# Kernel tuning notes

Measured on AMD Instinct MI355X. Metric: run time of the kernel, lower is better.

The kernel has to match this reference:

```python
import jax, jax.numpy as jnp
import numpy as np
import math

Z_DIM = 1024
DOWN = 512
UP = 1024
HEADS = 16
ROPE_HD = 64
HEAD_DIM = Z_DIM // HEADS  # 64, used only in softmax scale
V_HD = UP // HEADS


def _rope(x, num_heads, head_dim, base=10000.0):
    # x: [bs, L, num_heads*head_dim] -> [bs, num_heads, L, head_dim]
    bs, L, _ = x.shape
    theta = 1.0 / (base ** (jnp.arange(0, head_dim, 2, dtype=jnp.float32) / head_dim))
    pe = jnp.arange(L, dtype=jnp.float32)[:, None] * theta[None, :]  # [L, hd/2]
    # NOTE: faithful to source, which stores sin(pos) in cos_pos and cos(pos) in sin_pos
    cos_pos = jnp.repeat(jnp.sin(pe), 2, axis=-1)  # [L, hd]
    sin_pos = jnp.repeat(jnp.cos(pe), 2, axis=-1)
    q = x.reshape(bs, L, num_heads, head_dim).transpose(0, 2, 1, 3)
    q2 = jnp.stack([-q[..., 1::2], q[..., ::2]], axis=-1).reshape(q.shape)
    return q * cos_pos + q2 * sin_pos


def setup_inputs() -> dict:
    key = jax.random.key(0)
    ks = jax.random.split(key, 20)
    B, S = 2, 2048
    s = lambda fan_in: 1.0 / math.sqrt(fan_in)
    d = {
        'query': jax.random.normal(ks[0], (B, S, Z_DIM), jnp.float32),
        'key': jax.random.normal(ks[1], (B, S, Z_DIM), jnp.float32),
        'value': jax.random.normal(ks[2], (B, S, Z_DIM), jnp.float32),
        'w_dkv': jax.random.uniform(ks[3], (Z_DIM, DOWN), jnp.float32, -s(Z_DIM), s(Z_DIM)),
        'b_dkv': jnp.zeros((DOWN,), jnp.float32),
        'w_uk': jax.random.uniform(ks[4], (DOWN, UP), jnp.float32, -s(DOWN), s(DOWN)),
        'b_uk': jnp.zeros((UP,), jnp.float32),
        'w_uv': jax.random.uniform(ks[5], (DOWN, UP), jnp.float32, -s(DOWN), s(DOWN)),
        'b_uv': jnp.zeros((UP,), jnp.float32),
        'w_dq': jax.random.uniform(ks[6], (Z_DIM, DOWN), jnp.float32, -s(Z_DIM), s(Z_DIM)),
        'b_dq': jnp.zeros((DOWN,), jnp.float32),
        'w_uq': jax.random.uniform(ks[7], (DOWN, UP), jnp.float32, -s(DOWN), s(DOWN)),
        'b_uq': jnp.zeros((UP,), jnp.float32),
        'w_qr': jax.random.uniform(ks[8], (DOWN, ROPE_HD * HEADS), jnp.float32, -s(DOWN), s(DOWN)),
        'b_qr': jnp.zeros((ROPE_HD * HEADS,), jnp.float32),
        'w_kr': jax.random.uniform(ks[9], (Z_DIM, ROPE_HD), jnp.float32, -s(Z_DIM), s(Z_DIM)),
        'b_kr': jnp.zeros((ROPE_HD,), jnp.float32),
        'w_fc': jax.random.uniform(ks[10], (HEADS * V_HD, Z_DIM), jnp.float32, -s(HEADS * V_HD), s(HEADS * V_HD)),
        'b_fc': jnp.zeros((Z_DIM,), jnp.float32),
    }
    return d


def reference(query, key, value, w_dkv, b_dkv, w_uk, b_uk, w_uv, b_uv,
              w_dq, b_dq, w_uq, b_uq, w_qr, b_qr, w_kr, b_kr, w_fc, b_fc):
    bs, S, _ = query.shape
    c_t_kv = key @ w_dkv + b_dkv                      # [B,S,down]
    k_t_c = c_t_kv @ w_uk + b_uk                      # [B,S,up]
    v_t_c = c_t_kv @ w_uv + b_uv                      # [B,S,up]
    c_t_q = query @ w_dq + b_dq                       # [B,S,down]
    q_t_c = c_t_q @ w_uq + b_uq                       # [B,S,up]
    q_t_r = _rope(c_t_q @ w_qr + b_qr, HEADS, ROPE_HD)  # [B,H,S,rope_hd]
    k_t_r = _rope(key @ w_kr + b_kr, 1, ROPE_HD)         # [B,1,S,rope_hd]

    q_t_c = q_t_c.reshape(bs, S, HEADS, V_HD).transpose(0, 2, 1, 3)  # [B,H,S,dc]
    q = jnp.concatenate([q_t_c, q_t_r], axis=-1)                      # [B,H,S,dc+dr]
    k_t_c = k_t_c.reshape(bs, S, HEADS, V_HD).transpose(0, 2, 1, 3)
    k = jnp.concatenate([k_t_c, jnp.broadcast_to(k_t_r, (bs, HEADS, S, ROPE_HD))], axis=-1)

    scores = jnp.einsum('bhqd,bhkd->bhqk', q, k)
    scale = math.sqrt(HEAD_DIM) + math.sqrt(ROPE_HD)
    attn = jax.nn.softmax(scores / scale, axis=-1)    # dropout is identity (eval / p=0)

    v = v_t_c.reshape(bs, S, HEADS, V_HD).transpose(0, 2, 1, 3)
    out = jnp.einsum('bhqk,bhkd->bhqd', attn, v)      # [B,H,S,v_hd]
    out = out.transpose(0, 2, 1, 3).reshape(bs, S, HEADS * V_HD)
    return out @ w_fc + b_fc
```

## Files before the change

### kernel.cpp

```cpp
#include <hip/hip_runtime.h>
#include <hip/hip_bf16.h>
#include <hip/hip_fp16.h>

typedef __attribute__((ext_vector_type(8))) short    bf16x8;
typedef __attribute__((ext_vector_type(4))) float    f32x4;
typedef __attribute__((ext_vector_type(4))) _Float16 f16x4;
typedef __attribute__((ext_vector_type(2))) __fp16   fp16x2_raw;

typedef const void __attribute__((address_space(1))) gvoid_t;
typedef void __attribute__((address_space(3)))       lvoid_t;

static __device__ __forceinline__ void gload_lds16(const void* g, void* l) {
    __builtin_amdgcn_global_load_lds((gvoid_t*)g, (lvoid_t*)l, 16, 0, 0);
}

static __device__ __forceinline__ short bfbits(float f) {
    union { __hip_bfloat16 h; short s; } u;
    u.h = __float2bfloat16(f);
    return u.s;
}

__global__ __launch_bounds__(256) void cvt_bf16_dual(const float* __restrict__ q,
                                                     const float* __restrict__ k,
                                                     __hip_bfloat16* __restrict__ qd,
                                                     __hip_bfloat16* __restrict__ kd, int n8) {
    int t = blockIdx.x * 256 + threadIdx.x;
    const float* src;
    __hip_bfloat16* dst;
    int i;
    if (t < n8)          { src = q; dst = qd; i = t; }
    else if (t < 2 * n8) { src = k; dst = kd; i = t - n8; }
    else return;
    float4 a = ((const float4*)src)[2 * i];
    float4 b = ((const float4*)src)[2 * i + 1];
    bf16x8 o;
    o[0] = bfbits(a.x); o[1] = bfbits(a.y); o[2] = bfbits(a.z); o[3] = bfbits(a.w);
    o[4] = bfbits(b.x); o[5] = bfbits(b.y); o[6] = bfbits(b.z); o[7] = bfbits(b.w);
    ((bf16x8*)dst)[i] = o;
}

struct TJob { const float* src; __hip_bfloat16* dst; int K, N, tx; };
struct TJobPack { TJob j[8]; int start[8]; };

__global__ __launch_bounds__(256) void transpose_cvt_batch(TJobPack P) {
    __shared__ __hip_bfloat16 tile[64][72];
    const int bid = blockIdx.x;
    int ji = 0;
#pragma unroll
    for (int k = 1; k < 8; ++k) if (bid >= P.start[k]) ji = k;
    const TJob J = P.j[ji];
    const int local = bid - P.start[ji];
    const int kb = (local % J.tx) * 64;
    const int nb = (local / J.tx) * 64;
    const int c  = threadIdx.x & 63;
    const int r0 = threadIdx.x >> 6;
    if (nb < J.N) {
#pragma unroll
        for (int i = 0; i < 16; ++i) {
            int r = r0 + i * 4;
            tile[r][c] = __float2bfloat16(J.src[(size_t)(kb + r) * J.N + nb + c]);
        }
        __syncthreads();
#pragma unroll
        for (int i = 0; i < 16; ++i) {
            int r = r0 + i * 4;
            J.dst[(size_t)(nb + r) * J.K + kb + c] = tile[c][r];
        }
    } else {
        __hip_bfloat16 z = __float2bfloat16(0.0f);
#pragma unroll
        for (int i = 0; i < 16; ++i) {
            int r = r0 + i * 4;
            J.dst[(size_t)(nb + r) * J.K + kb + c] = z;
        }
    }
}

__global__ __launch_bounds__(256) void bias_prep(const float* __restrict__ b_dkv, const float* __restrict__ b_kr,
                                                 const float* __restrict__ b_uk,  const float* __restrict__ b_uv,
                                                 const float* __restrict__ b_uq,  const float* __restrict__ b_qr,
                                                 float* __restrict__ bcat1, float* __restrict__ bcat2,
                                                 float* __restrict__ bcat3) {
    int t = blockIdx.x * 256 + threadIdx.x;
    if (t < 640) {
        bcat1[t] = (t < 512) ? b_dkv[t] : ((t - 512) < 64 ? b_kr[t - 512] : 0.0f);
    } else if (t < 2688) {
        int u = t - 640;
        bcat2[u] = (u < 1024) ? b_uq[u] : b_qr[u - 1024];
    } else if (t < 4736) {
        int u = t - 2688;
        bcat3[u] = (u < 1024) ? b_uk[u] : b_uv[u - 1024];
    }
}

struct GJob {
    const __hip_bfloat16* A; const __hip_bfloat16* Bt; const float* bias;
    void* C0; void* C1; int N, K, lda, ldb, ldc; float scale; int mode;
};

__global__ __launch_bounds__(256) void gemm_dual(GJob j0, GJob j1, int split) {
    __shared__ __align__(16) __hip_bfloat16 sA[2][64 * 32];
    __shared__ __align__(16) __hip_bfloat16 sB[2][128 * 32];
    const GJob J  = (blockIdx.x < (unsigned)split) ? j0 : j1;
    const int bx  = (blockIdx.x < (unsigned)split) ? blockIdx.x : blockIdx.x - split;
    const int tid  = threadIdx.x;
    const int wid  = tid >> 6;
    const int lane = tid & 63;
    const int lr   = lane & 15;
    const int lg   = lane >> 4;
    const int mb   = blockIdx.y * 64;
    const int nb   = bx * 128;
    const int wr   = (wid >> 1) * 32;
    const int wc   = (wid & 1) * 64;

    auto stage = [&](int bufi, int k0) {
        {
            int e   = wid * 512 + lane * 8;
            int row = e >> 5, col = e & 31;
            gload_lds16(J.A + (size_t)(mb + row) * J.lda + (k0 + col), &sA[bufi][wid * 512]);
        }
#pragma unroll
        for (int j = 0; j < 2; ++j) {
            int cb  = wid * 2 + j;
            int e   = cb * 512 + lane * 8;
            int row = e >> 5, col = e & 31;
            gload_lds16(J.Bt + (size_t)(nb + row) * J.ldb + (k0 + col), &sB[bufi][cb * 512]);
        }
    };

    f32x4 acc[2][4] = {};
    const int nt = J.K / 32;
    stage(0, 0);
    asm volatile("s_waitcnt vmcnt(0)" ::: "memory");
    __syncthreads();

    for (int t = 0; t < nt; ++t) {
        const int cur = t & 1;
        if (t + 1 < nt) stage(cur ^ 1, (t + 1) * 32);
        bf16x8 af[2], bfr[4];
#pragma unroll
        for (int m = 0; m < 2; ++m)
            af[m] = *(const bf16x8*)&sA[cur][(wr + m * 16 + lr) * 32 + lg * 8];
#pragma unroll
        for (int n = 0; n < 4; ++n)
            bfr[n] = *(const bf16x8*)&sB[cur][(wc + n * 16 + lr) * 32 + lg * 8];
#pragma unroll
        for (int m = 0; m < 2; ++m)
#pragma unroll
            for (int n = 0; n < 4; ++n)
                acc[m][n] = __builtin_amdgcn_mfma_f32_16x16x32_bf16(af[m], bfr[n], acc[m][n], 0, 0, 0);
        asm volatile("s_waitcnt vmcnt(0)" ::: "memory");
        __syncthreads();
    }

#pragma unroll
    for (int n = 0; n < 4; ++n) {
        int col  = nb + wc + n * 16 + lr;
        float bv = J.bias ? J.bias[col] : 0.0f;
#pragma unroll
        for (int m = 0; m < 2; ++m) {
#pragma unroll
            for (int r = 0; r < 4; ++r) {
                int row    = mb + wr + m * 16 + lg * 4 + r;
                float val  = (acc[m][n][r] + bv) * J.scale;
                if (J.mode == 1) ((float*)J.C0)[(size_t)row * J.ldc + col] = val;
                else             ((__hip_bfloat16*)J.C0)[(size_t)row * J.ldc + col] = __float2bfloat16(val);
            }
        }
    }
}

__global__ __launch_bounds__(256) void gemm128_dual(GJob j0, GJob j1, int split) {
    __shared__ __align__(16) __hip_bfloat16 sA[2][128 * 32];
    __shared__ __align__(16) __hip_bfloat16 sB[2][128 * 32];
    const GJob J  = (blockIdx.x < (unsigned)split) ? j0 : j1;
    const int bx  = (blockIdx.x < (unsigned)split) ? blockIdx.x : blockIdx.x - split;
    const int tid  = threadIdx.x;
    const int wid  = tid >> 6;
    const int lane = tid & 63;
    const int lr   = lane & 15;
    const int lg   = lane >> 4;
    const int mb   = blockIdx.y * 128;
    const int nb   = bx * 128;
    const int wr   = (wid >> 1) * 64;
    const int wc   = (wid & 1) * 64;

    auto stage = [&](int bufi, int k0) {
#pragma unroll
        for (int j = 0; j < 2; ++j) {
            int c   = wid * 2 + j;
            int e   = c * 512 + lane * 8;
            int row = e >> 5, col = e & 31;
            gload_lds16(J.A + (size_t)(mb + row) * J.lda + (k0 + col), &sA[bufi][c * 512]);
        }
#pragma unroll
        for (int j = 0; j < 2; ++j) {
            int c   = wid * 2 + j;
            int e   = c * 512 + lane * 8;
            int row = e >> 5, col = e & 31;
            gload_lds16(J.Bt + (size_t)(nb + row) * J.ldb + (k0 + col), &sB[bufi][c * 512]);
        }
    };

    f32x4 acc[4][4] = {};
    const int nt = J.K / 32;
    stage(0, 0);
    asm volatile("s_waitcnt vmcnt(0)" ::: "memory");
    __syncthreads();

    for (int t = 0; t < nt; ++t) {
        const int cur = t & 1;
        if (t + 1 < nt) stage(cur ^ 1, (t + 1) * 32);
        bf16x8 af[4], bfr[4];
#pragma unroll
        for (int m = 0; m < 4; ++m)
            af[m] = *(const bf16x8*)&sA[cur][(wr + m * 16 + lr) * 32 + lg * 8];
#pragma unroll
        for (int n = 0; n < 4; ++n)
            bfr[n] = *(const bf16x8*)&sB[cur][(wc + n * 16 + lr) * 32 + lg * 8];
#pragma unroll
        for (int m = 0; m < 4; ++m)
#pragma unroll
            for (int n = 0; n < 4; ++n)
                acc[m][n] = __builtin_amdgcn_mfma_f32_16x16x32_bf16(af[m], bfr[n], acc[m][n], 0, 0, 0);
        asm volatile("s_waitcnt vmcnt(0)" ::: "memory");
        __syncthreads();
    }

#pragma unroll
    for (int n = 0; n < 4; ++n) {
        int col  = nb + wc + n * 16 + lr;
        float bv = J.bias ? J.bias[col] : 0.0f;
#pragma unroll
        for (int m = 0; m < 4; ++m) {
#pragma unroll
            for (int r = 0; r < 4; ++r) {
                int row    = mb + wr + m * 16 + lg * 4 + r;
                float val  = (acc[m][n][r] + bv) * J.scale;
                if (J.mode == 3) {
                    if (col < 1024) ((__hip_bfloat16*)J.C0)[(size_t)row * 1024 + col] = __float2bfloat16(val);
                    else            ((_Float16*)J.C1)[(size_t)row * 1024 + col - 1024] = (_Float16)val;
                } else {
                    ((__hip_bfloat16*)J.C0)[(size_t)row * J.ldc + col] = __float2bfloat16(val);
                }
            }
        }
    }
}

__global__ __launch_bounds__(256) void misc_kernel(const _Float16* __restrict__ vtc,
                                                   _Float16* __restrict__ vtcT,
                                                   __hip_bfloat16* __restrict__ qrope,
                                                   __hip_bfloat16* __restrict__ krope,
                                                   int R, int S) {
    __shared__ _Float16 tile[64][72];
    const int tp  = R >> 2;
    const int bid = blockIdx.x;
    if (bid < tp) {
        const int cb = (bid % 16) * 64;
        const int rb = (bid / 16) * 64;
        const int c4 = (threadIdx.x & 15) * 4;
        const int rl = threadIdx.x >> 4;
#pragma unroll
        for (int i = 0; i < 4; ++i) {
            int row = rl + i * 16;
            *(f16x4*)&tile[row][c4] = *(const f16x4*)&vtc[(size_t)(rb + row) * 1024 + cb + c4];
        }
        __syncthreads();
#pragma unroll
        for (int i = 0; i < 4; ++i) {
            int orow = rl + i * 16;
            f16x4 v;
#pragma unroll
            for (int j = 0; j < 4; ++j) v[j] = tile[c4 + j][orow];
            *(f16x4*)&vtcT[(size_t)(cb + orow) * R + rb + c4] = v;
        }
        return;
    }
    int t = (bid - tp) * 256 + threadIdx.x;
    const int nq = R * 512;
    __hip_bfloat16* x;
    int i, row, rowstride, hh;
    if (t < nq)               { i = t & 31; hh = (t >> 5) & 15; row = t >> 9; x = qrope; rowstride = 2048; }
    else if (t < nq + R * 32) { t -= nq; i = t & 31; hh = 0; row = t >> 5; x = krope; rowstride = 640; }
    else return;
    int pos = row % S;
    float theta = __expf(-0.28782313662425572f * (float)i);
    float pe = (float)pos * theta;
    float sp, cp;
    sincosf(pe, &sp, &cp);
    size_t idx = (size_t)row * rowstride + hh * 64 + 2 * i;
    float x0 = __bfloat162float(x[idx]);
    float x1 = __bfloat162float(x[idx + 1]);
    x[idx]     = __float2bfloat16(x0 * sp - x1 * cp);
    x[idx + 1] = __float2bfloat16(x1 * sp + x0 * cp);
}

__global__ __launch_bounds__(256, 2) void attn_kernel(const __hip_bfloat16* __restrict__ qcat,
                                                      const __hip_bfloat16* __restrict__ ktc,
                                                      const __hip_bfloat16* __restrict__ kr,
                                                      const _Float16* __restrict__ vtcT,
                                                      __hip_bfloat16* __restrict__ outp,
                                                      int S, int R) {
    __shared__ __align__(16) char lds[2][24 * 1024];
    const int tid  = threadIdx.x;
    const int wid  = tid >> 6;
    const int lane = tid & 63;
    const int lr   = lane & 15;
    const int lg   = lane >> 4;

    const int NQ   = S / 128;
    const int L    = blockIdx.x;
    const int slot = L >> 3;
    const int gg   = (L & 7) + 8 * (slot / NQ);
    const int qt   = slot % NQ;
    const int h    = gg & 15;
    const int b    = gg >> 4;
    const size_t base = (size_t)b * S;
    const int qb   = qt * 128 + wid * 32;

    auto stage = [&](int bufi, int kt) {
        char* bufK = lds[bufi];
        char* bufV = lds[bufi] + 16 * 1024;
#pragma unroll
        for (int j = 0; j < 4; ++j) {
            int c   = wid * 4 + j;
            int rho = c * 4 + (lane >> 4);
            int u   = (lane & 15) ^ (rho & 15);
            const __hip_bfloat16* src = (u < 8)
                ? ktc + (base + kt + rho) * 1024 + h * 64 + u * 8
                : kr  + (base + kt + rho) * 640 + (u & 7) * 8;
            gload_lds16(src, bufK + c * 1024);
        }
#pragma unroll
        for (int j = 0; j < 2; ++j) {
            int c   = wid * 2 + j;
            int rho = c * 8 + (lane >> 3);
            int u   = (lane & 7) ^ (rho & 7);
            gload_lds16(vtcT + (size_t)(h * 64 + rho) * R + base + kt + u * 8,
                        bufV + c * 1024);
        }
    };

    bf16x8 qf[2][4];
#pragma unroll
    for (int g = 0; g < 2; ++g) {
        size_t row = base + qb + g * 16 + lr;
        const __hip_bfloat16* pq = qcat + row * 2048 + h * 64;
        qf[g][0] = *(const bf16x8*)(pq + lg * 8);
        qf[g][1] = *(const bf16x8*)(pq + 32 + lg * 8);
        qf[g][2] = *(const bf16x8*)(pq + 1024 + lg * 8);
        qf[g][3] = *(const bf16x8*)(pq + 1024 + 32 + lg * 8);
    }

    f32x4 oacc[2][4] = {};
    float lrun[2] = {0.0f, 0.0f};

    const int NT = S / 64;
    stage(0, 0);
    __syncthreads();

    for (int t = 0; t < NT; ++t) {
        const int cur = t & 1;
        if (t + 1 < NT) stage(cur ^ 1, (t + 1) * 64);

        const char* bufK = lds[cur];
        const char* bufV = lds[cur] + 16 * 1024;

        f32x4 sacc[2][4] = {};
#pragma unroll
        for (int st = 0; st < 4; ++st) {
            bf16x8 kf[4];
#pragma unroll
            for (int c = 0; c < 4; ++c)
                kf[c] = *(const bf16x8*)(bufK + (st * 16 + lr) * 256 +
                                         (((c * 4 + lg) ^ lr) << 4));
#pragma unroll
            for (int g = 0; g < 2; ++g)
#pragma unroll
                for (int c = 0; c < 4; ++c)
                    sacc[g][st] = __builtin_amdgcn_mfma_f32_16x16x32_bf16(kf[c], qf[g][c], sacc[g][st], 0, 0, 0);
        }

        f16x4 vf[4][4];
#pragma unroll
        for (int st = 0; st < 4; ++st)
#pragma unroll
            for (int vt = 0; vt < 4; ++vt)
                vf[st][vt] = *(const f16x4*)(bufV + (vt * 16 + lr) * 128 +
                                             (((st * 2 + (lg >> 1)) ^ (lr & 7)) << 4) + (lg & 1) * 8);

#pragma unroll
        for (int g = 0; g < 2; ++g) {
            float p[4][4];
#pragma unroll
            for (int st = 0; st < 4; ++st)
#pragma unroll
                for (int r = 0; r < 4; ++r) {
                    p[st][r] = __builtin_exp2f(sacc[g][st][r]);
                    lrun[g] += p[st][r];
                }
#pragma unroll
            for (int st = 0; st < 4; ++st) {
                union { fp16x2_raw h2[2]; f16x4 v; } pu;
                pu.h2[0] = __builtin_amdgcn_cvt_pkrtz(p[st][0], p[st][1]);
                pu.h2[1] = __builtin_amdgcn_cvt_pkrtz(p[st][2], p[st][3]);
#pragma unroll
                for (int vt = 0; vt < 4; ++vt)
                    oacc[g][vt] = __builtin_amdgcn_mfma_f32_16x16x16f16(vf[st][vt], pu.v, oacc[g][vt], 0, 0, 0);
            }
        }
        __syncthreads();
    }

#pragma unroll
    for (int g = 0; g < 2; ++g) {
        lrun[g] += __shfl_xor(lrun[g], 16);
        lrun[g] += __shfl_xor(lrun[g], 32);
        float inv = 1.0f / lrun[g];
        size_t rowoff = (base + qb + g * 16 + lr) << 10;
#pragma unroll
        for (int vt = 0; vt < 4; ++vt)
#pragma unroll
            for (int r = 0; r < 4; ++r)
                outp[rowoff + h * 64 + vt * 16 + lg * 4 + r] =
                    __float2bfloat16(oacc[g][vt][r] * inv);
    }
}

extern "C" void kernel_launch(void* const* d_in, const int* in_sizes, int n_in,
                              void* d_out, int out_size, void* d_ws, size_t ws_size,
                              hipStream_t stream) {
    const float* query = (const float*)d_in[0];
    const float* key   = (const float*)d_in[1];
    const float* w_dkv = (const float*)d_in[3];
    const float* b_dkv = (const float*)d_in[4];
    const float* w_uk  = (const float*)d_in[5];
    const float* b_uk  = (const float*)d_in[6];
    const float* w_uv  = (const float*)d_in[7];
    const float* b_uv  = (const float*)d_in[8];
    const float* w_dq  = (const float*)d_in[9];
    const float* b_dq  = (const float*)d_in[10];
    const float* w_uq  = (const float*)d_in[11];
    const float* b_uq  = (const float*)d_in[12];
    const float* w_qr  = (const float*)d_in[13];
    const float* b_qr  = (const float*)d_in[14];
    const float* w_kr  = (const float*)d_in[15];
    const float* b_kr  = (const float*)d_in[16];
    const float* w_fc  = (const float*)d_in[17];
    const float* b_fc  = (const float*)d_in[18];

    const int B = 2;
    const int R = in_sizes[0] / 1024;
    const int S = R / B;
    const float QSCALE = 1.4426950408889634f / 16.0f;

    char* ws = (char*)d_ws;
    size_t off = 0;
    auto alloc = [&](size_t bytes) -> char* {
        char* p = ws + off;
        off += (bytes + 255) & ~(size_t)255;
        return p;
    };

    __hip_bfloat16* q_bf  = (__hip_bfloat16*)alloc((size_t)R * 1024 * 2);
    __hip_bfloat16* k_bf  = (__hip_bfloat16*)alloc((size_t)R * 1024 * 2);
    __hip_bfloat16* wcat1 = (__hip_bfloat16*)alloc(640 * 1024 * 2);
    __hip_bfloat16* wdq_t = (__hip_bfloat16*)alloc(512 * 1024 * 2);
    __hip_bfloat16* wcat3 = (__hip_bfloat16*)alloc(2048 * 512 * 2);
    __hip_bfloat16* wcat2 = (__hip_bfloat16*)alloc(2048 * 512 * 2);
    __hip_bfloat16* wfc_t = (__hip_bfloat16*)alloc(1024 * 1024 * 2);
    float*          bcat1 = (float*)alloc(640 * 4);
    float*          bcat2 = (float*)alloc(2048 * 4);
    float*          bcat3 = (float*)alloc(2048 * 4);
    __hip_bfloat16* ckkr  = (__hip_bfloat16*)alloc((size_t)R * 640 * 2);
    __hip_bfloat16* c_q   = (__hip_bfloat16*)alloc((size_t)R * 512 * 2);
    __hip_bfloat16* ktc   = (__hip_bfloat16*)alloc((size_t)R * 1024 * 2);
    _Float16*       vtc   = (_Float16*)alloc((size_t)R * 1024 * 2);
    _Float16*       vtcT  = (_Float16*)alloc((size_t)R * 1024 * 2);
    __hip_bfloat16* qcat  = (__hip_bfloat16*)alloc((size_t)R * 2048 * 2);
    __hip_bfloat16* attn_out = q_bf;

    cvt_bf16_dual<<<dim3(2 * R * 1024 / 8 / 256), 256, 0, stream>>>(query, key, q_bf, k_bf, R * 1024 / 8);

    TJobPack P;
    P.j[0] = {w_dkv, wcat1,              1024, 512,  16};
    P.j[1] = {w_kr,  wcat1 + 512 * 1024, 1024, 64,   16};
    P.j[2] = {w_dq,  wdq_t,              1024, 512,  16};
    P.j[3] = {w_uk,  wcat3,              512,  1024, 8};
    P.j[4] = {w_uv,  wcat3 + 1024 * 512, 512,  1024, 8};
    P.j[5] = {w_uq,  wcat2,              512,  1024, 8};
    P.j[6] = {w_qr,  wcat2 + 1024 * 512, 512,  1024, 8};
    P.j[7] = {w_fc,  wfc_t,              1024, 1024, 16};
    int st = 0;
    const int counts[8] = {128, 32, 128, 128, 128, 128, 128, 256};
    for (int i = 0; i < 8; ++i) { P.start[i] = st; st += counts[i]; }
    transpose_cvt_batch<<<dim3(st), 256, 0, stream>>>(P);

    bias_prep<<<dim3(19), 256, 0, stream>>>(b_dkv, b_kr, b_uk, b_uv, b_uq, b_qr, bcat1, bcat2, bcat3);

    GJob ja0 = {k_bf, wcat1, bcat1, ckkr, nullptr, 640, 1024, 1024, 1024, 640, 1.0f, 0};
    GJob ja1 = {q_bf, wdq_t, b_dq,  c_q,  nullptr, 512, 1024, 1024, 1024, 512, 1.0f, 0};
    gemm_dual<<<dim3(9, R / 64), 256, 0, stream>>>(ja0, ja1, 5);

    GJob jb0 = {ckkr, wcat3, bcat3, ktc,  vtc,     2048, 512, 640, 512, 1024, 1.0f,   3};
    GJob jb1 = {c_q,  wcat2, bcat2, qcat, nullptr, 2048, 512, 512, 512, 2048, QSCALE, 0};
    gemm128_dual<<<dim3(32, R / 128), 256, 0, stream>>>(jb0, jb1, 16);

    {
        int tp = R >> 2;
        int ropeBlocks = (R * 512 + R * 32 + 255) / 256;
        misc_kernel<<<dim3(tp + ropeBlocks), 256, 0, stream>>>(vtc, vtcT, qcat + 1024, ckkr + 512, R, S);
    }

    attn_kernel<<<dim3((S / 128) * 16 * B), 256, 0, stream>>>(qcat, ktc, ckkr + 512, vtcT, attn_out, S, R);

    GJob jc0 = {attn_out, wfc_t, b_fc, d_out, nullptr, 1024, 1024, 1024, 1024, 1024, 1.0f, 1};
    gemm_dual<<<dim3(8, R / 64), 256, 0, stream>>>(jc0, jc0, 8);
}
```

Measured before the change: 187.7 us.

## Fuse V transpose into up-projection GEMM epilogue via LDS staging

The up-projection GEMM now transposes the V output tile through shared memory in its epilogue and writes vtcT directly with vectorized stores. This removes the intermediate vtc buffer and the transpose part of the misc kernel, saving one full read and write of V. The rope kernel also switches to fast __sincosf and a bitmask for the position, assuming S is a power of two. The fast sincos may lose some accuracy for large arguments.

```diff
diff --git a/kernel.cpp b/kernel.cpp
--- a/kernel.cpp
+++ b/kernel.cpp
@@ -5,6 +5,7 @@
 typedef __attribute__((ext_vector_type(8))) short    bf16x8;
 typedef __attribute__((ext_vector_type(4))) float    f32x4;
 typedef __attribute__((ext_vector_type(4))) _Float16 f16x4;
+typedef __attribute__((ext_vector_type(8))) _Float16 f16x8;
 typedef __attribute__((ext_vector_type(2))) __fp16   fp16x2_raw;
 
 typedef const void __attribute__((address_space(1))) gvoid_t;
@@ -170,9 +171,10 @@
     }
 }
 
-__global__ __launch_bounds__(256) void gemm128_dual(GJob j0, GJob j1, int split) {
-    __shared__ __align__(16) __hip_bfloat16 sA[2][128 * 32];
-    __shared__ __align__(16) __hip_bfloat16 sB[2][128 * 32];
+__global__ __launch_bounds__(256) void gemm128_dual(GJob j0, GJob j1, int split, int Rtot) {
+    __shared__ __align__(16) char smem[128 * 132 * 2];
+    __hip_bfloat16* sA = (__hip_bfloat16*)smem;
+    __hip_bfloat16* sB = (__hip_bfloat16*)(smem + 16384);
     const GJob J  = (blockIdx.x < (unsigned)split) ? j0 : j1;
     const int bx  = (blockIdx.x < (unsigned)split) ? blockIdx.x : blockIdx.x - split;
     const int tid  = threadIdx.x;
@@ -191,14 +193,14 @@
             int c   = wid * 2 + j;
             int e   = c * 512 + lane * 8;
             int row = e >> 5, col = e & 31;
-            gload_lds16(J.A + (size_t)(mb + row) * J.lda + (k0 + col), &sA[bufi][c * 512]);
+            gload_lds16(J.A + (size_t)(mb + row) * J.lda + (k0 + col), &sA[bufi * 4096 + c * 512]);
         }
 #pragma unroll
         for (int j = 0; j < 2; ++j) {
             int c   = wid * 2 + j;
             int e   = c * 512 + lane * 8;
             int row = e >> 5, col = e & 31;
-            gload_lds16(J.Bt + (size_t)(nb + row) * J.ldb + (k0 + col), &sB[bufi][c * 512]);
+            gload_lds16(J.Bt + (size_t)(nb + row) * J.ldb + (k0 + col), &sB[bufi * 4096 + c * 512]);
         }
     };
 
@@ -214,10 +216,10 @@
         bf16x8 af[4], bfr[4];
 #pragma unroll
         for (int m = 0; m < 4; ++m)
-            af[m] = *(const bf16x8*)&sA[cur][(wr + m * 16 + lr) * 32 + lg * 8];
+            af[m] = *(const bf16x8*)&sA[cur * 4096 + (wr + m * 16 + lr) * 32 + lg * 8];
 #pragma unroll
         for (int n = 0; n < 4; ++n)
-            bfr[n] = *(const bf16x8*)&sB[cur][(wc + n * 16 + lr) * 32 + lg * 8];
+            bfr[n] = *(const bf16x8*)&sB[cur * 4096 + (wc + n * 16 + lr) * 32 + lg * 8];
 #pragma unroll
         for (int m = 0; m < 4; ++m)
 #pragma unroll
@@ -227,6 +229,30 @@
         __syncthreads();
     }
 
+    if (J.mode == 3 && nb >= 1024) {
+        _Float16* T = (_Float16*)smem;
+#pragma unroll
+        for (int n = 0; n < 4; ++n) {
+            int cl = wc + n * 16 + lr;
+            float bv = J.bias[nb + cl];
+#pragma unroll
+            for (int m = 0; m < 4; ++m)
+#pragma unroll
+                for (int r = 0; r < 4; ++r)
+                    T[cl * 132 + wr + m * 16 + lg * 4 + r] =
+                        (_Float16)((acc[m][n][r] + bv) * J.scale);
+        }
+        __syncthreads();
+        const int vd   = tid >> 1;
+        const int half = tid & 1;
+        _Float16* dst = (_Float16*)J.C1 + (size_t)(nb - 1024 + vd) * Rtot + mb + half * 64;
+        const _Float16* srcT = T + vd * 132 + half * 64;
+#pragma unroll
+        for (int j = 0; j < 8; ++j)
+            *(f16x8*)&dst[j * 8] = *(const f16x8*)&srcT[j * 8];
+        return;
+    }
+
 #pragma unroll
     for (int n = 0; n < 4; ++n) {
         int col  = nb + wc + n * 16 + lr;
@@ -237,58 +263,28 @@
             for (int r = 0; r < 4; ++r) {
                 int row    = mb + wr + m * 16 + lg * 4 + r;
                 float val  = (acc[m][n][r] + bv) * J.scale;
-                if (J.mode == 3) {
-                    if (col < 1024) ((__hip_bfloat16*)J.C0)[(size_t)row * 1024 + col] = __float2bfloat16(val);
-                    else            ((_Float16*)J.C1)[(size_t)row * 1024 + col - 1024] = (_Float16)val;
-                } else {
-                    ((__hip_bfloat16*)J.C0)[(size_t)row * J.ldc + col] = __float2bfloat16(val);
-                }
+                if (J.mode == 3) ((__hip_bfloat16*)J.C0)[(size_t)row * 1024 + col] = __float2bfloat16(val);
+                else             ((__hip_bfloat16*)J.C0)[(size_t)row * J.ldc + col] = __float2bfloat16(val);
             }
         }
     }
 }
 
-__global__ __launch_bounds__(256) void misc_kernel(const _Float16* __restrict__ vtc,
-                                                   _Float16* __restrict__ vtcT,
-                                                   __hip_bfloat16* __restrict__ qrope,
+__global__ __launch_bounds__(256) void rope_kernel(__hip_bfloat16* __restrict__ qrope,
                                                    __hip_bfloat16* __restrict__ krope,
                                                    int R, int S) {
-    __shared__ _Float16 tile[64][72];
-    const int tp  = R >> 2;
-    const int bid = blockIdx.x;
-    if (bid < tp) {
-        const int cb = (bid % 16) * 64;
-        const int rb = (bid / 16) * 64;
-        const int c4 = (threadIdx.x & 15) * 4;
-        const int rl = threadIdx.x >> 4;
-#pragma unroll
-        for (int i = 0; i < 4; ++i) {
-            int row = rl + i * 16;
-            *(f16x4*)&tile[row][c4] = *(const f16x4*)&vtc[(size_t)(rb + row) * 1024 + cb + c4];
-        }
-        __syncthreads();
-#pragma unroll
-        for (int i = 0; i < 4; ++i) {
-            int orow = rl + i * 16;
-            f16x4 v;
-#pragma unroll
-            for (int j = 0; j < 4; ++j) v[j] = tile[c4 + j][orow];
-            *(f16x4*)&vtcT[(size_t)(cb + orow) * R + rb + c4] = v;
-        }
-        return;
-    }
-    int t = (bid - tp) * 256 + threadIdx.x;
+    int t = blockIdx.x * 256 + threadIdx.x;
     const int nq = R * 512;
     __hip_bfloat16* x;
     int i, row, rowstride, hh;
     if (t < nq)               { i = t & 31; hh = (t >> 5) & 15; row = t >> 9; x = qrope; rowstride = 2048; }
     else if (t < nq + R * 32) { t -= nq; i = t & 31; hh = 0; row = t >> 5; x = krope; rowstride = 640; }
     else return;
-    int pos = row % S;
+    int pos = row & (S - 1);
     float theta = __expf(-0.28782313662425572f * (float)i);
     float pe = (float)pos * theta;
     float sp, cp;
-    sincosf(pe, &sp, &cp);
+    __sincosf(pe, &sp, &cp);
     size_t idx = (size_t)row * rowstride + hh * 64 + 2 * i;
     float x0 = __bfloat162float(x[idx]);
     float x1 = __bfloat162float(x[idx + 1]);
@@ -476,7 +472,6 @@
     __hip_bfloat16* ckkr  = (__hip_bfloat16*)alloc((size_t)R * 640 * 2);
     __hip_bfloat16* c_q   = (__hip_bfloat16*)alloc((size_t)R * 512 * 2);
     __hip_bfloat16* ktc   = (__hip_bfloat16*)alloc((size_t)R * 1024 * 2);
-    _Float16*       vtc   = (_Float16*)alloc((size_t)R * 1024 * 2);
     _Float16*       vtcT  = (_Float16*)alloc((size_t)R * 1024 * 2);
     __hip_bfloat16* qcat  = (__hip_bfloat16*)alloc((size_t)R * 2048 * 2);
     __hip_bfloat16* attn_out = q_bf;
@@ -503,15 +498,11 @@
     GJob ja1 = {q_bf, wdq_t, b_dq,  c_q,  nullptr, 512, 1024, 1024, 1024, 512, 1.0f, 0};
     gemm_dual<<<dim3(9, R / 64), 256, 0, stream>>>(ja0, ja1, 5);
 
-    GJob jb0 = {ckkr, wcat3, bcat3, ktc,  vtc,     2048, 512, 640, 512, 1024, 1.0f,   3};
+    GJob jb0 = {ckkr, wcat3, bcat3, ktc,  vtcT,    2048, 512, 640, 512, 1024, 1.0f,   3};
     GJob jb1 = {c_q,  wcat2, bcat2, qcat, nullptr, 2048, 512, 512, 512, 2048, QSCALE, 0};
-    gemm128_dual<<<dim3(32, R / 128), 256, 0, stream>>>(jb0, jb1, 16);
-
-    {
-        int tp = R >> 2;
-        int ropeBlocks = (R * 512 + R * 32 + 255) / 256;
-        misc_kernel<<<dim3(tp + ropeBlocks), 256, 0, stream>>>(vtc, vtcT, qcat + 1024, ckkr + 512, R, S);
-    }
+    gemm128_dual<<<dim3(32, R / 128), 256, 0, stream>>>(jb0, jb1, 16, R);
+
+    rope_kernel<<<dim3((R * 512 + R * 32 + 255) / 256), 256, 0, stream>>>(qcat + 1024, ckkr + 512, R, S);
 
     attn_kernel<<<dim3((S / 128) * 16 * B), 256, 0, stream>>>(qcat, ktc, ckkr + 512, vtcT, attn_out, S, R);
 
```

Measured after the change: 181.0 us. -3.6%, faster.
